# Performance work log

Measured on AMD Instinct MI355X. Metric: run time of the kernel, lower is better.

Reference implementation:

```python
import jax, jax.numpy as jnp
import numpy as np

B, L, V, D = 8, 2048, 1024, 512  # batch, seq (max_len), vocab_size (input feat), embedding_dim

def setup_inputs() -> dict:
    key = jax.random.key(0)
    kx, kq, kk, kv = jax.random.split(key, 4)
    scale = 1.0 / np.sqrt(V)
    return {
        "x": jax.random.normal(kx, (B, L, V), dtype=jnp.float32),
        "Wq": jax.random.uniform(kq, (D, V), dtype=jnp.float32, minval=-scale, maxval=scale),
        "Wk": jax.random.uniform(kk, (D, V), dtype=jnp.float32, minval=-scale, maxval=scale),
        "Wv": jax.random.uniform(kv, (D, V), dtype=jnp.float32, minval=-scale, maxval=scale),
    }

def reference(x, Wq, Wk, Wv):
    # nn.Linear without bias: y = x @ W.T
    q = jnp.einsum('blv,dv->bld', x, Wq)
    k = jnp.einsum('blv,dv->bld', x, Wk)
    v = jnp.einsum('blv,dv->bld', x, Wv)
    scores = jnp.einsum('bqd,bkd->bqk', q, k) / jnp.sqrt(jnp.float32(D))
    attn = jax.nn.softmax(scores, axis=2)
    return jnp.einsum('bqk,bkd->bqd', attn, v)
```

## Files before the change

### kernel.cpp

```cpp
#include <hip/hip_runtime.h>
#include <cstdint>
#include <cstddef>


typedef __attribute__((ext_vector_type(8))) __bf16 bf16x8;
typedef __attribute__((ext_vector_type(16))) float f32x16;
typedef __attribute__((ext_vector_type(4))) unsigned short ushort4v;
typedef __attribute__((ext_vector_type(4))) unsigned int uint4v;

__device__ __forceinline__ unsigned short f2bf(float f) {
  unsigned u = __float_as_uint(f);
  return (unsigned short)((u + 0x7fffu + ((u >> 16) & 1u)) >> 16);
}

__device__ __forceinline__ void async_load16(const unsigned short* g, unsigned short* l) {
  __builtin_amdgcn_global_load_lds(
      (__attribute__((address_space(1))) void*)(g),
      (__attribute__((address_space(3))) void*)(l), 16, 0, 0);
}

__global__ __launch_bounds__(256) void cvt_f32_bf16(const float* __restrict__ src,
                                                    unsigned short* __restrict__ dst) {
  int i = (blockIdx.x * 256 + threadIdx.x) * 4;
  float4 v = *(const float4*)(src + i);
  ushort4v o;
  o.x = f2bf(v.x); o.y = f2bf(v.y); o.z = f2bf(v.z); o.w = f2bf(v.w);
  *(ushort4v*)(dst + i) = o;
}

__global__ __launch_bounds__(256) void cvt_w3(const float* __restrict__ a,
                                              const float* __restrict__ b,
                                              const float* __restrict__ c,
                                              unsigned short* __restrict__ dst) {
  int bx = blockIdx.x;
  const float* src = (bx < 512) ? a : (bx < 1024) ? b : c;
  int seg = (bx < 512) ? 0 : (bx < 1024) ? 1 : 2;
  int i = ((bx & 511) * 256 + threadIdx.x) * 4;
  float4 v = *(const float4*)(src + i);
  ushort4v o;
  o.x = f2bf(v.x); o.y = f2bf(v.y); o.z = f2bf(v.z); o.w = f2bf(v.w);
  *(ushort4v*)(dst + seg * 524288 + i) = o;
}

__global__ __launch_bounds__(256) void gemm_qkv(
    const unsigned short* __restrict__ A0,
    const unsigned short* __restrict__ Bw,
    unsigned short* __restrict__ qk,
    unsigned short* __restrict__ vT) {
  __shared__ unsigned short sA[128 * 64];
  __shared__ unsigned short sB[128 * 64];
  const int tid = threadIdx.x;
  const int lane = tid & 63, wid = tid >> 6;
  const int wm = wid & 1, wn = wid >> 1;
  const int l31 = lane & 31, half = lane >> 5;

  int flat = blockIdx.x + blockIdx.y * 12;
  int sub = flat >> 3;
  int bxp = sub % 12;
  int byp = (flat & 7) * 16 + sub / 12;

  const unsigned short* A = A0 + (size_t)byp * 128 * 1024;
  const unsigned short* B = Bw + (size_t)bxp * 128 * 1024;

  f32x16 acc[2][2] = {};

  for (int k0 = 0; k0 < 1024; k0 += 64) {
    __syncthreads();
    #pragma unroll
    for (int p = 0; p < 4; ++p) {
      int u = p * 256 + tid;
      int r = u >> 3, cs = (u & 7) ^ (r & 7);
      async_load16(&A[(size_t)r * 1024 + k0 + cs * 8], &sA[u * 8]);
      async_load16(&B[(size_t)r * 1024 + k0 + cs * 8], &sB[u * 8]);
    }
    __syncthreads();

    #pragma unroll
    for (int ks = 0; ks < 4; ++ks) {
      int cb = ks * 2 + half;
      bf16x8 aF[2], bF[2];
      #pragma unroll
      for (int i = 0; i < 2; ++i) {
        int rA = wm * 64 + i * 32 + l31;
        aF[i] = *(const bf16x8*)&sA[(rA * 8 + (cb ^ (rA & 7))) * 8];
        int rB = wn * 64 + i * 32 + l31;
        bF[i] = *(const bf16x8*)&sB[(rB * 8 + (cb ^ (rB & 7))) * 8];
      }
      #pragma unroll
      for (int mt = 0; mt < 2; ++mt)
        #pragma unroll
        for (int nt = 0; nt < 2; ++nt)
          acc[mt][nt] = __builtin_amdgcn_mfma_f32_32x32x16_bf16(
              aF[mt], bF[nt], acc[mt][nt], 0, 0, 0);
    }
  }

  if (bxp < 8) {
    unsigned short* Cc = qk + (size_t)byp * 128 * 1024 + (size_t)bxp * 128;
    #pragma unroll
    for (int mt = 0; mt < 2; ++mt)
      #pragma unroll
      for (int nt = 0; nt < 2; ++nt) {
        int col = wn * 64 + nt * 32 + l31;
        #pragma unroll
        for (int q = 0; q < 4; ++q) {
          int row = wm * 64 + mt * 32 + half * 4 + q * 8;
          #pragma unroll
          for (int r2 = 0; r2 < 4; ++r2)
            Cc[(size_t)(row + r2) * 1024 + col] = f2bf(acc[mt][nt][q * 4 + r2]);
        }
      }
  } else {
    int nvx = bxp - 8;
    #pragma unroll
    for (int mt = 0; mt < 2; ++mt)
      #pragma unroll
      for (int nt = 0; nt < 2; ++nt) {
        int d = nvx * 128 + wn * 64 + nt * 32 + l31;
        #pragma unroll
        for (int q = 0; q < 4; ++q) {
          int grow = byp * 128 + wm * 64 + mt * 32 + half * 4 + q * 8;
          int b = grow >> 11, l = grow & 2047;
          ushort4v o;
          o.x = f2bf(acc[mt][nt][q * 4 + 0]); o.y = f2bf(acc[mt][nt][q * 4 + 1]);
          o.z = f2bf(acc[mt][nt][q * 4 + 2]); o.w = f2bf(acc[mt][nt][q * 4 + 3]);
          *(ushort4v*)&vT[(size_t)b * 1048576 + (size_t)d * 2048 + l] = o;
        }
      }
  }
}

__global__ __launch_bounds__(256) void gemm_exp(
    const unsigned short* __restrict__ qk,
    unsigned short* __restrict__ S, float scale) {
  __shared__ unsigned short sA[128 * 64];
  __shared__ unsigned short sB[128 * 64];
  const int tid = threadIdx.x;
  const int lane = tid & 63, wid = tid >> 6;
  const int wm = wid & 1, wn = wid >> 1;
  const int l31 = lane & 31, half = lane >> 5;

  int flat = blockIdx.x + (blockIdx.y << 4) + (blockIdx.z << 8);
  int z = flat & 7, rem = flat >> 3;
  int bxp = rem & 15, byp = rem >> 4;

  const unsigned short* A  = qk + (size_t)z * 2097152 + (size_t)byp * 128 * 1024;
  const unsigned short* Bk = qk + 512 + (size_t)z * 2097152 + (size_t)bxp * 128 * 1024;

  f32x16 acc[2][2] = {};

  for (int k0 = 0; k0 < 512; k0 += 64) {
    __syncthreads();
    #pragma unroll
    for (int p = 0; p < 4; ++p) {
      int u = p * 256 + tid;
      int r = u >> 3, cs = (u & 7) ^ (r & 7);
      async_load16(&A[(size_t)r * 1024 + k0 + cs * 8], &sA[u * 8]);
      async_load16(&Bk[(size_t)r * 1024 + k0 + cs * 8], &sB[u * 8]);
    }
    __syncthreads();

    #pragma unroll
    for (int ks = 0; ks < 4; ++ks) {
      int cb = ks * 2 + half;
      bf16x8 aF[2], bF[2];
      #pragma unroll
      for (int i = 0; i < 2; ++i) {
        int rA = wm * 64 + i * 32 + l31;
        aF[i] = *(const bf16x8*)&sA[(rA * 8 + (cb ^ (rA & 7))) * 8];
        int rB = wn * 64 + i * 32 + l31;
        bF[i] = *(const bf16x8*)&sB[(rB * 8 + (cb ^ (rB & 7))) * 8];
      }
      #pragma unroll
      for (int mt = 0; mt < 2; ++mt)
        #pragma unroll
        for (int nt = 0; nt < 2; ++nt)
          acc[mt][nt] = __builtin_amdgcn_mfma_f32_32x32x16_bf16(
              aF[mt], bF[nt], acc[mt][nt], 0, 0, 0);
    }
  }

  unsigned short* Cc = S + (size_t)z * 4194304 +
                       (size_t)byp * 128 * 2048 + (size_t)bxp * 128;
  #pragma unroll
  for (int mt = 0; mt < 2; ++mt)
    #pragma unroll
    for (int nt = 0; nt < 2; ++nt) {
      int col = wn * 64 + nt * 32 + l31;
      #pragma unroll
      for (int q = 0; q < 4; ++q) {
        int row = wm * 64 + mt * 32 + half * 4 + q * 8;
        #pragma unroll
        for (int r2 = 0; r2 < 4; ++r2)
          Cc[(size_t)(row + r2) * 2048 + col] =
              f2bf(__expf(acc[mt][nt][q * 4 + r2] * scale));
      }
    }
}

__global__ __launch_bounds__(256) void gemm_pvT(
    const unsigned short* __restrict__ S, const unsigned short* __restrict__ vT,
    float* __restrict__ out) {
  __shared__ unsigned short sA[128 * 64];
  __shared__ unsigned short sB[128 * 64];
  const int tid = threadIdx.x;
  const int lane = tid & 63, wid = tid >> 6;
  const int wm = wid & 1, wn = wid >> 1;
  const int l31 = lane & 31, half = lane >> 5;

  int flat = blockIdx.x + (blockIdx.y << 2) + (blockIdx.z << 6);
  int b = flat & 7, rem = flat >> 3;
  int dblk = rem & 3, qblk = rem >> 2;

  const unsigned short* A  = vT + (size_t)b * 1048576 + (size_t)dblk * 128 * 2048;
  const unsigned short* Bs = S  + (size_t)b * 4194304 + (size_t)qblk * 128 * 2048;

  f32x16 acc[2][2] = {};
  float rsum[2] = {0.f, 0.f};

  for (int k0 = 0; k0 < 2048; k0 += 64) {
    __syncthreads();
    #pragma unroll
    for (int p = 0; p < 4; ++p) {
      int u = p * 256 + tid;
      int r = u >> 3, cs = (u & 7) ^ (r & 7);
      async_load16(&A[(size_t)r * 2048 + k0 + cs * 8], &sA[u * 8]);
      async_load16(&Bs[(size_t)r * 2048 + k0 + cs * 8], &sB[u * 8]);
    }
    __syncthreads();

    #pragma unroll
    for (int ks = 0; ks < 4; ++ks) {
      int cb = ks * 2 + half;
      bf16x8 aF[2], bF[2];
      #pragma unroll
      for (int i = 0; i < 2; ++i) {
        int rA = wm * 64 + i * 32 + l31;
        aF[i] = *(const bf16x8*)&sA[(rA * 8 + (cb ^ (rA & 7))) * 8];
        int rB = wn * 64 + i * 32 + l31;
        bF[i] = *(const bf16x8*)&sB[(rB * 8 + (cb ^ (rB & 7))) * 8];
      }
      #pragma unroll
      for (int i = 0; i < 2; ++i) {
        uint4v u = __builtin_bit_cast(uint4v, bF[i]);
        #pragma unroll
        for (int t = 0; t < 4; ++t)
          rsum[i] += __uint_as_float(u[t] << 16) +
                     __uint_as_float(u[t] & 0xffff0000u);
      }
      #pragma unroll
      for (int mt = 0; mt < 2; ++mt)
        #pragma unroll
        for (int nt = 0; nt < 2; ++nt)
          acc[mt][nt] = __builtin_amdgcn_mfma_f32_32x32x16_bf16(
              aF[mt], bF[nt], acc[mt][nt], 0, 0, 0);
    }
  }

  #pragma unroll
  for (int i = 0; i < 2; ++i) rsum[i] += __shfl_xor(rsum[i], 32, 64);

  #pragma unroll
  for (int nt = 0; nt < 2; ++nt) {
    float inv = __builtin_amdgcn_rcpf(rsum[nt]);
    int qpos = qblk * 128 + wn * 64 + nt * 32 + l31;
    #pragma unroll
    for (int mt = 0; mt < 2; ++mt) {
      int d0 = dblk * 128 + wm * 64 + mt * 32 + half * 4;
      float* op = out + ((size_t)b * 2048 + qpos) * 512 + d0;
      #pragma unroll
      for (int q = 0; q < 4; ++q) {
        float4 o;
        o.x = acc[mt][nt][q * 4 + 0] * inv;
        o.y = acc[mt][nt][q * 4 + 1] * inv;
        o.z = acc[mt][nt][q * 4 + 2] * inv;
        o.w = acc[mt][nt][q * 4 + 3] * inv;
        *(float4*)(op + q * 8) = o;
      }
    }
  }
}

extern "C" void kernel_launch(void* const* d_in, const int* in_sizes, int n_in,
                              void* d_out, int out_size, void* d_ws, size_t ws_size,
                              hipStream_t stream) {
  const float* x  = (const float*)d_in[0];
  const float* Wq = (const float*)d_in[1];
  const float* Wk = (const float*)d_in[2];
  const float* Wv = (const float*)d_in[3];
  float* out = (float*)d_out;
  char* ws = (char*)d_ws;

  unsigned short* xb = (unsigned short*)ws;
  unsigned short* S  = (unsigned short*)ws;
  unsigned short* wf = (unsigned short*)(ws + 33554432);
  unsigned short* qk = (unsigned short*)(ws + 67108864);
  unsigned short* vT = (unsigned short*)(ws + 100663296);

  const float rsqrtD = 0.044194173824159216f;

  hipLaunchKernelGGL(cvt_f32_bf16, dim3(16384), dim3(256), 0, stream, x, xb);
  hipLaunchKernelGGL(cvt_w3, dim3(1536), dim3(256), 0, stream, Wq, Wk, Wv, wf);

  hipLaunchKernelGGL(gemm_qkv, dim3(12, 128, 1), dim3(256), 0, stream, xb, wf, qk, vT);

  hipLaunchKernelGGL(gemm_exp, dim3(16, 16, 8), dim3(256), 0, stream, qk, S, rsqrtD);

  hipLaunchKernelGGL(gemm_pvT, dim3(4, 16, 8), dim3(256), 0, stream, S, vT, out);

  (void)in_sizes; (void)n_in; (void)out_size; (void)ws_size;
}
```

Measured before the change: 267.6 us.

## Fuse all attention stages into one persistent cooperative kernel with grid syncs

Replaces the five separate launches (conversion, QKV GEMM, QK^T+exp, PV) with a single cooperative persistent kernel. Blocks loop over the tiles of each stage, with grid.sync between stages. The aim is to remove launch gaps and the tail effects between kernels. In exchange, the grid is capped at up to 768 blocks with launch_bounds(256,3), which may lower occupancy, and per-stage tiles are spread less evenly. The pvT stage has only 512 tiles, so some blocks sit idle there.

```diff
diff --git a/kernel.cpp b/kernel.cpp
--- a/kernel.cpp
+++ b/kernel.cpp
@@ -1,6 +1,9 @@
 #include <hip/hip_runtime.h>
+#include <hip/hip_cooperative_groups.h>
 #include <cstdint>
 #include <cstddef>
+
+namespace cg = cooperative_groups;
 
 
 typedef __attribute__((ext_vector_type(8))) __bf16 bf16x8;
@@ -18,6 +21,291 @@
       (__attribute__((address_space(1))) void*)(g),
       (__attribute__((address_space(3))) void*)(l), 16, 0, 0);
 }
+
+
+__device__ __forceinline__ void cvt_unit(int u0, const float* __restrict__ x,
+                                         const float* __restrict__ Wq,
+                                         const float* __restrict__ Wk,
+                                         const float* __restrict__ Wv,
+                                         unsigned short* __restrict__ xb,
+                                         unsigned short* __restrict__ wf, int tid) {
+  const float* src;
+  unsigned short* dst;
+  int i;
+  if (u0 < 16384) {
+    i = (u0 * 256 + tid) * 4;
+    src = x; dst = xb;
+  } else {
+    int bx = u0 - 16384;
+    src = (bx < 512) ? Wq : (bx < 1024) ? Wk : Wv;
+    int seg = (bx < 512) ? 0 : (bx < 1024) ? 1 : 2;
+    i = ((bx & 511) * 256 + tid) * 4;
+    dst = wf + seg * 524288;
+  }
+  float4 v = *(const float4*)(src + i);
+  ushort4v o;
+  o.x = f2bf(v.x); o.y = f2bf(v.y); o.z = f2bf(v.z); o.w = f2bf(v.w);
+  *(ushort4v*)(dst + i) = o;
+}
+
+__device__ __forceinline__ void qkv_tile(int flat, const unsigned short* __restrict__ A0,
+                                         const unsigned short* __restrict__ Bw,
+                                         unsigned short* __restrict__ qk,
+                                         unsigned short* __restrict__ vT,
+                                         unsigned short* sA, unsigned short* sB, int tid) {
+  const int lane = tid & 63, wid = tid >> 6;
+  const int wm = wid & 1, wn = wid >> 1;
+  const int l31 = lane & 31, half = lane >> 5;
+
+  int sub = flat >> 3;
+  int bxp = sub % 12;
+  int byp = (flat & 7) * 16 + sub / 12;
+
+  const unsigned short* A = A0 + (size_t)byp * 128 * 1024;
+  const unsigned short* B = Bw + (size_t)bxp * 128 * 1024;
+
+  f32x16 acc[2][2] = {};
+
+  for (int k0 = 0; k0 < 1024; k0 += 64) {
+    __syncthreads();
+    #pragma unroll
+    for (int p = 0; p < 4; ++p) {
+      int u = p * 256 + tid;
+      int r = u >> 3, cs = (u & 7) ^ (r & 7);
+      async_load16(&A[(size_t)r * 1024 + k0 + cs * 8], &sA[u * 8]);
+      async_load16(&B[(size_t)r * 1024 + k0 + cs * 8], &sB[u * 8]);
+    }
+    __syncthreads();
+
+    #pragma unroll
+    for (int ks = 0; ks < 4; ++ks) {
+      int cb = ks * 2 + half;
+      bf16x8 aF[2], bF[2];
+      #pragma unroll
+      for (int i = 0; i < 2; ++i) {
+        int rA = wm * 64 + i * 32 + l31;
+        aF[i] = *(const bf16x8*)&sA[(rA * 8 + (cb ^ (rA & 7))) * 8];
+        int rB = wn * 64 + i * 32 + l31;
+        bF[i] = *(const bf16x8*)&sB[(rB * 8 + (cb ^ (rB & 7))) * 8];
+      }
+      #pragma unroll
+      for (int mt = 0; mt < 2; ++mt)
+        #pragma unroll
+        for (int nt = 0; nt < 2; ++nt)
+          acc[mt][nt] = __builtin_amdgcn_mfma_f32_32x32x16_bf16(
+              aF[mt], bF[nt], acc[mt][nt], 0, 0, 0);
+    }
+  }
+
+  if (bxp < 8) {
+    unsigned short* Cc = qk + (size_t)byp * 128 * 1024 + (size_t)bxp * 128;
+    #pragma unroll
+    for (int mt = 0; mt < 2; ++mt)
+      #pragma unroll
+      for (int nt = 0; nt < 2; ++nt) {
+        int col = wn * 64 + nt * 32 + l31;
+        #pragma unroll
+        for (int q = 0; q < 4; ++q) {
+          int row = wm * 64 + mt * 32 + half * 4 + q * 8;
+          #pragma unroll
+          for (int r2 = 0; r2 < 4; ++r2)
+            Cc[(size_t)(row + r2) * 1024 + col] = f2bf(acc[mt][nt][q * 4 + r2]);
+        }
+      }
+  } else {
+    int nvx = bxp - 8;
+    #pragma unroll
+    for (int mt = 0; mt < 2; ++mt)
+      #pragma unroll
+      for (int nt = 0; nt < 2; ++nt) {
+        int d = nvx * 128 + wn * 64 + nt * 32 + l31;
+        #pragma unroll
+        for (int q = 0; q < 4; ++q) {
+          int grow = byp * 128 + wm * 64 + mt * 32 + half * 4 + q * 8;
+          int b = grow >> 11, l = grow & 2047;
+          ushort4v o;
+          o.x = f2bf(acc[mt][nt][q * 4 + 0]); o.y = f2bf(acc[mt][nt][q * 4 + 1]);
+          o.z = f2bf(acc[mt][nt][q * 4 + 2]); o.w = f2bf(acc[mt][nt][q * 4 + 3]);
+          *(ushort4v*)&vT[(size_t)b * 1048576 + (size_t)d * 2048 + l] = o;
+        }
+      }
+  }
+}
+
+__device__ __forceinline__ void exp_tile(int flat, const unsigned short* __restrict__ qk,
+                                         unsigned short* __restrict__ S,
+                                         unsigned short* sA, unsigned short* sB, int tid) {
+  const float scale = 0.044194173824159216f;
+  const int lane = tid & 63, wid = tid >> 6;
+  const int wm = wid & 1, wn = wid >> 1;
+  const int l31 = lane & 31, half = lane >> 5;
+
+  int z = flat & 7, rem = flat >> 3;
+  int bxp = rem & 15, byp = rem >> 4;
+
+  const unsigned short* A  = qk + (size_t)z * 2097152 + (size_t)byp * 128 * 1024;
+  const unsigned short* Bk = qk + 512 + (size_t)z * 2097152 + (size_t)bxp * 128 * 1024;
+
+  f32x16 acc[2][2] = {};
+
+  for (int k0 = 0; k0 < 512; k0 += 64) {
+    __syncthreads();
+    #pragma unroll
+    for (int p = 0; p < 4; ++p) {
+      int u = p * 256 + tid;
+      int r = u >> 3, cs = (u & 7) ^ (r & 7);
+      async_load16(&A[(size_t)r * 1024 + k0 + cs * 8], &sA[u * 8]);
+      async_load16(&Bk[(size_t)r * 1024 + k0 + cs * 8], &sB[u * 8]);
+    }
+    __syncthreads();
+
+    #pragma unroll
+    for (int ks = 0; ks < 4; ++ks) {
+      int cb = ks * 2 + half;
+      bf16x8 aF[2], bF[2];
+      #pragma unroll
+      for (int i = 0; i < 2; ++i) {
+        int rA = wm * 64 + i * 32 + l31;
+        aF[i] = *(const bf16x8*)&sA[(rA * 8 + (cb ^ (rA & 7))) * 8];
+        int rB = wn * 64 + i * 32 + l31;
+        bF[i] = *(const bf16x8*)&sB[(rB * 8 + (cb ^ (rB & 7))) * 8];
+      }
+      #pragma unroll
+      for (int mt = 0; mt < 2; ++mt)
+        #pragma unroll
+        for (int nt = 0; nt < 2; ++nt)
+          acc[mt][nt] = __builtin_amdgcn_mfma_f32_32x32x16_bf16(
+              aF[mt], bF[nt], acc[mt][nt], 0, 0, 0);
+    }
+  }
+
+  unsigned short* Cc = S + (size_t)z * 4194304 +
+                       (size_t)byp * 128 * 2048 + (size_t)bxp * 128;
+  #pragma unroll
+  for (int mt = 0; mt < 2; ++mt)
+    #pragma unroll
+    for (int nt = 0; nt < 2; ++nt) {
+      int col = wn * 64 + nt * 32 + l31;
+      #pragma unroll
+      for (int q = 0; q < 4; ++q) {
+        int row = wm * 64 + mt * 32 + half * 4 + q * 8;
+        #pragma unroll
+        for (int r2 = 0; r2 < 4; ++r2)
+          Cc[(size_t)(row + r2) * 2048 + col] =
+              f2bf(__expf(acc[mt][nt][q * 4 + r2] * scale));
+      }
+    }
+}
+
+__device__ __forceinline__ void pvT_tile(int flat, const unsigned short* __restrict__ S,
+                                         const unsigned short* __restrict__ vT,
+                                         float* __restrict__ out,
+                                         unsigned short* sA, unsigned short* sB, int tid) {
+  const int lane = tid & 63, wid = tid >> 6;
+  const int wm = wid & 1, wn = wid >> 1;
+  const int l31 = lane & 31, half = lane >> 5;
+
+  int b = flat & 7, rem = flat >> 3;
+  int dblk = rem & 3, qblk = rem >> 2;
+
+  const unsigned short* A  = vT + (size_t)b * 1048576 + (size_t)dblk * 128 * 2048;
+  const unsigned short* Bs = S  + (size_t)b * 4194304 + (size_t)qblk * 128 * 2048;
+
+  f32x16 acc[2][2] = {};
+  float rsum[2] = {0.f, 0.f};
+
+  for (int k0 = 0; k0 < 2048; k0 += 64) {
+    __syncthreads();
+    #pragma unroll
+    for (int p = 0; p < 4; ++p) {
+      int u = p * 256 + tid;
+      int r = u >> 3, cs = (u & 7) ^ (r & 7);
+      async_load16(&A[(size_t)r * 2048 + k0 + cs * 8], &sA[u * 8]);
+      async_load16(&Bs[(size_t)r * 2048 + k0 + cs * 8], &sB[u * 8]);
+    }
+    __syncthreads();
+
+    #pragma unroll
+    for (int ks = 0; ks < 4; ++ks) {
+      int cb = ks * 2 + half;
+      bf16x8 aF[2], bF[2];
+      #pragma unroll
+      for (int i = 0; i < 2; ++i) {
+        int rA = wm * 64 + i * 32 + l31;
+        aF[i] = *(const bf16x8*)&sA[(rA * 8 + (cb ^ (rA & 7))) * 8];
+        int rB = wn * 64 + i * 32 + l31;
+        bF[i] = *(const bf16x8*)&sB[(rB * 8 + (cb ^ (rB & 7))) * 8];
+      }
+      #pragma unroll
+      for (int i = 0; i < 2; ++i) {
+        uint4v u = __builtin_bit_cast(uint4v, bF[i]);
+        #pragma unroll
+        for (int t = 0; t < 4; ++t)
+          rsum[i] += __uint_as_float(u[t] << 16) +
+                     __uint_as_float(u[t] & 0xffff0000u);
+      }
+      #pragma unroll
+      for (int mt = 0; mt < 2; ++mt)
+        #pragma unroll
+        for (int nt = 0; nt < 2; ++nt)
+          acc[mt][nt] = __builtin_amdgcn_mfma_f32_32x32x16_bf16(
+              aF[mt], bF[nt], acc[mt][nt], 0, 0, 0);
+    }
+  }
+
+  #pragma unroll
+  for (int i = 0; i < 2; ++i) rsum[i] += __shfl_xor(rsum[i], 32, 64);
+
+  #pragma unroll
+  for (int nt = 0; nt < 2; ++nt) {
+    float inv = __builtin_amdgcn_rcpf(rsum[nt]);
+    int qpos = qblk * 128 + wn * 64 + nt * 32 + l31;
+    #pragma unroll
+    for (int mt = 0; mt < 2; ++mt) {
+      int d0 = dblk * 128 + wm * 64 + mt * 32 + half * 4;
+      float* op = out + ((size_t)b * 2048 + qpos) * 512 + d0;
+      #pragma unroll
+      for (int q = 0; q < 4; ++q) {
+        float4 o;
+        o.x = acc[mt][nt][q * 4 + 0] * inv;
+        o.y = acc[mt][nt][q * 4 + 1] * inv;
+        o.z = acc[mt][nt][q * 4 + 2] * inv;
+        o.w = acc[mt][nt][q * 4 + 3] * inv;
+        *(float4*)(op + q * 8) = o;
+      }
+    }
+  }
+}
+
+
+__global__ __launch_bounds__(256, 3) void fused_attn(
+    const float* __restrict__ x, const float* __restrict__ Wq,
+    const float* __restrict__ Wk, const float* __restrict__ Wv,
+    float* __restrict__ out, char* __restrict__ ws) {
+  __shared__ unsigned short sA[128 * 64];
+  __shared__ unsigned short sB[128 * 64];
+  unsigned short* xb = (unsigned short*)ws;
+  unsigned short* S  = (unsigned short*)ws;
+  unsigned short* wf = (unsigned short*)(ws + 33554432);
+  unsigned short* qk = (unsigned short*)(ws + 67108864);
+  unsigned short* vT = (unsigned short*)(ws + 100663296);
+  const int tid = threadIdx.x;
+  const int G = gridDim.x;
+  cg::grid_group grid = cg::this_grid();
+
+  for (int u = blockIdx.x; u < 17920; u += G)
+    cvt_unit(u, x, Wq, Wk, Wv, xb, wf, tid);
+  grid.sync();
+  for (int t = blockIdx.x; t < 1536; t += G)
+    qkv_tile(t, xb, wf, qk, vT, sA, sB, tid);
+  grid.sync();
+  for (int t = blockIdx.x; t < 2048; t += G)
+    exp_tile(t, qk, S, sA, sB, tid);
+  grid.sync();
+  for (int t = blockIdx.x; t < 512; t += G)
+    pvT_tile(t, S, vT, out, sA, sB, tid);
+}
+
 
 __global__ __launch_bounds__(256) void cvt_f32_bf16(const float* __restrict__ src,
                                                     unsigned short* __restrict__ dst) {
@@ -43,159 +331,18 @@
 }
 
 __global__ __launch_bounds__(256) void gemm_qkv(
-    const unsigned short* __restrict__ A0,
-    const unsigned short* __restrict__ Bw,
-    unsigned short* __restrict__ qk,
-    unsigned short* __restrict__ vT) {
+    const unsigned short* __restrict__ A0, const unsigned short* __restrict__ Bw,
+    unsigned short* __restrict__ qk, unsigned short* __restrict__ vT) {
   __shared__ unsigned short sA[128 * 64];
   __shared__ unsigned short sB[128 * 64];
-  const int tid = threadIdx.x;
-  const int lane = tid & 63, wid = tid >> 6;
-  const int wm = wid & 1, wn = wid >> 1;
-  const int l31 = lane & 31, half = lane >> 5;
-
-  int flat = blockIdx.x + blockIdx.y * 12;
-  int sub = flat >> 3;
-  int bxp = sub % 12;
-  int byp = (flat & 7) * 16 + sub / 12;
-
-  const unsigned short* A = A0 + (size_t)byp * 128 * 1024;
-  const unsigned short* B = Bw + (size_t)bxp * 128 * 1024;
-
-  f32x16 acc[2][2] = {};
-
-  for (int k0 = 0; k0 < 1024; k0 += 64) {
-    __syncthreads();
-    #pragma unroll
-    for (int p = 0; p < 4; ++p) {
-      int u = p * 256 + tid;
-      int r = u >> 3, cs = (u & 7) ^ (r & 7);
-      async_load16(&A[(size_t)r * 1024 + k0 + cs * 8], &sA[u * 8]);
-      async_load16(&B[(size_t)r * 1024 + k0 + cs * 8], &sB[u * 8]);
-    }
-    __syncthreads();
-
-    #pragma unroll
-    for (int ks = 0; ks < 4; ++ks) {
-      int cb = ks * 2 + half;
-      bf16x8 aF[2], bF[2];
-      #pragma unroll
-      for (int i = 0; i < 2; ++i) {
-        int rA = wm * 64 + i * 32 + l31;
-        aF[i] = *(const bf16x8*)&sA[(rA * 8 + (cb ^ (rA & 7))) * 8];
-        int rB = wn * 64 + i * 32 + l31;
-        bF[i] = *(const bf16x8*)&sB[(rB * 8 + (cb ^ (rB & 7))) * 8];
-      }
-      #pragma unroll
-      for (int mt = 0; mt < 2; ++mt)
-        #pragma unroll
-        for (int nt = 0; nt < 2; ++nt)
-          acc[mt][nt] = __builtin_amdgcn_mfma_f32_32x32x16_bf16(
-              aF[mt], bF[nt], acc[mt][nt], 0, 0, 0);
-    }
-  }
-
-  if (bxp < 8) {
-    unsigned short* Cc = qk + (size_t)byp * 128 * 1024 + (size_t)bxp * 128;
-    #pragma unroll
-    for (int mt = 0; mt < 2; ++mt)
-      #pragma unroll
-      for (int nt = 0; nt < 2; ++nt) {
-        int col = wn * 64 + nt * 32 + l31;
-        #pragma unroll
-        for (int q = 0; q < 4; ++q) {
-          int row = wm * 64 + mt * 32 + half * 4 + q * 8;
-          #pragma unroll
-          for (int r2 = 0; r2 < 4; ++r2)
-            Cc[(size_t)(row + r2) * 1024 + col] = f2bf(acc[mt][nt][q * 4 + r2]);
-        }
-      }
-  } else {
-    int nvx = bxp - 8;
-    #pragma unroll
-    for (int mt = 0; mt < 2; ++mt)
-      #pragma unroll
-      for (int nt = 0; nt < 2; ++nt) {
-        int d = nvx * 128 + wn * 64 + nt * 32 + l31;
-        #pragma unroll
-        for (int q = 0; q < 4; ++q) {
-          int grow = byp * 128 + wm * 64 + mt * 32 + half * 4 + q * 8;
-          int b = grow >> 11, l = grow & 2047;
-          ushort4v o;
-          o.x = f2bf(acc[mt][nt][q * 4 + 0]); o.y = f2bf(acc[mt][nt][q * 4 + 1]);
-          o.z = f2bf(acc[mt][nt][q * 4 + 2]); o.w = f2bf(acc[mt][nt][q * 4 + 3]);
-          *(ushort4v*)&vT[(size_t)b * 1048576 + (size_t)d * 2048 + l] = o;
-        }
-      }
-  }
+  qkv_tile(blockIdx.x + blockIdx.y * 12, A0, Bw, qk, vT, sA, sB, threadIdx.x);
 }
 
 __global__ __launch_bounds__(256) void gemm_exp(
-    const unsigned short* __restrict__ qk,
-    unsigned short* __restrict__ S, float scale) {
+    const unsigned short* __restrict__ qk, unsigned short* __restrict__ S) {
   __shared__ unsigned short sA[128 * 64];
   __shared__ unsigned short sB[128 * 64];
-  const int tid = threadIdx.x;
-  const int lane = tid & 63, wid = tid >> 6;
-  const int wm = wid & 1, wn = wid >> 1;
-  const int l31 = lane & 31, half = lane >> 5;
-
-  int flat = blockIdx.x + (blockIdx.y << 4) + (blockIdx.z << 8);
-  int z = flat & 7, rem = flat >> 3;
-  int bxp = rem & 15, byp = rem >> 4;
-
-  const unsigned short* A  = qk + (size_t)z * 2097152 + (size_t)byp * 128 * 1024;
-  const unsigned short* Bk = qk + 512 + (size_t)z * 2097152 + (size_t)bxp * 128 * 1024;
-
-  f32x16 acc[2][2] = {};
-
-  for (int k0 = 0; k0 < 512; k0 += 64) {
-    __syncthreads();
-    #pragma unroll
-    for (int p = 0; p < 4; ++p) {
-      int u = p * 256 + tid;
-      int r = u >> 3, cs = (u & 7) ^ (r & 7);
-      async_load16(&A[(size_t)r * 1024 + k0 + cs * 8], &sA[u * 8]);
-      async_load16(&Bk[(size_t)r * 1024 + k0 + cs * 8], &sB[u * 8]);
-    }
-    __syncthreads();
-
-    #pragma unroll
-    for (int ks = 0; ks < 4; ++ks) {
-      int cb = ks * 2 + half;
-      bf16x8 aF[2], bF[2];
-      #pragma unroll
-      for (int i = 0; i < 2; ++i) {
-        int rA = wm * 64 + i * 32 + l31;
-        aF[i] = *(const bf16x8*)&sA[(rA * 8 + (cb ^ (rA & 7))) * 8];
-        int rB = wn * 64 + i * 32 + l31;
-        bF[i] = *(const bf16x8*)&sB[(rB * 8 + (cb ^ (rB & 7))) * 8];
-      }
-      #pragma unroll
-      for (int mt = 0; mt < 2; ++mt)
-        #pragma unroll
-        for (int nt = 0; nt < 2; ++nt)
-          acc[mt][nt] = __builtin_amdgcn_mfma_f32_32x32x16_bf16(
-              aF[mt], bF[nt], acc[mt][nt], 0, 0, 0);
-    }
-  }
-
-  unsigned short* Cc = S + (size_t)z * 4194304 +
-                       (size_t)byp * 128 * 2048 + (size_t)bxp * 128;
-  #pragma unroll
-  for (int mt = 0; mt < 2; ++mt)
-    #pragma unroll
-    for (int nt = 0; nt < 2; ++nt) {
-      int col = wn * 64 + nt * 32 + l31;
-      #pragma unroll
-      for (int q = 0; q < 4; ++q) {
-        int row = wm * 64 + mt * 32 + half * 4 + q * 8;
-        #pragma unroll
-        for (int r2 = 0; r2 < 4; ++r2)
-          Cc[(size_t)(row + r2) * 2048 + col] =
-              f2bf(__expf(acc[mt][nt][q * 4 + r2] * scale));
-      }
-    }
+  exp_tile(blockIdx.x + (blockIdx.y << 4) + (blockIdx.z << 8), qk, S, sA, sB, threadIdx.x);
 }
 
 __global__ __launch_bounds__(256) void gemm_pvT(
@@ -203,82 +350,7 @@
     float* __restrict__ out) {
   __shared__ unsigned short sA[128 * 64];
   __shared__ unsigned short sB[128 * 64];
-  const int tid = threadIdx.x;
-  const int lane = tid & 63, wid = tid >> 6;
-  const int wm = wid & 1, wn = wid >> 1;
-  const int l31 = lane & 31, half = lane >> 5;
-
-  int flat = blockIdx.x + (blockIdx.y << 2) + (blockIdx.z << 6);
-  int b = flat & 7, rem = flat >> 3;
-  int dblk = rem & 3, qblk = rem >> 2;
-
-  const unsigned short* A  = vT + (size_t)b * 1048576 + (size_t)dblk * 128 * 2048;
-  const unsigned short* Bs = S  + (size_t)b * 4194304 + (size_t)qblk * 128 * 2048;
-
-  f32x16 acc[2][2] = {};
-  float rsum[2] = {0.f, 0.f};
-
-  for (int k0 = 0; k0 < 2048; k0 += 64) {
-    __syncthreads();
-    #pragma unroll
-    for (int p = 0; p < 4; ++p) {
-      int u = p * 256 + tid;
-      int r = u >> 3, cs = (u & 7) ^ (r & 7);
-      async_load16(&A[(size_t)r * 2048 + k0 + cs * 8], &sA[u * 8]);
-      async_load16(&Bs[(size_t)r * 2048 + k0 + cs * 8], &sB[u * 8]);
-    }
-    __syncthreads();
-
-    #pragma unroll
-    for (int ks = 0; ks < 4; ++ks) {
-      int cb = ks * 2 + half;
-      bf16x8 aF[2], bF[2];
-      #pragma unroll
-      for (int i = 0; i < 2; ++i) {
-        int rA = wm * 64 + i * 32 + l31;
-        aF[i] = *(const bf16x8*)&sA[(rA * 8 + (cb ^ (rA & 7))) * 8];
-        int rB = wn * 64 + i * 32 + l31;
-        bF[i] = *(const bf16x8*)&sB[(rB * 8 + (cb ^ (rB & 7))) * 8];
-      }
-      #pragma unroll
-      for (int i = 0; i < 2; ++i) {
-        uint4v u = __builtin_bit_cast(uint4v, bF[i]);
-        #pragma unroll
-        for (int t = 0; t < 4; ++t)
-          rsum[i] += __uint_as_float(u[t] << 16) +
-                     __uint_as_float(u[t] & 0xffff0000u);
-      }
-      #pragma unroll
-      for (int mt = 0; mt < 2; ++mt)
-        #pragma unroll
-        for (int nt = 0; nt < 2; ++nt)
-          acc[mt][nt] = __builtin_amdgcn_mfma_f32_32x32x16_bf16(
-              aF[mt], bF[nt], acc[mt][nt], 0, 0, 0);
-    }
-  }
-
-  #pragma unroll
-  for (int i = 0; i < 2; ++i) rsum[i] += __shfl_xor(rsum[i], 32, 64);
-
-  #pragma unroll
-  for (int nt = 0; nt < 2; ++nt) {
-    float inv = __builtin_amdgcn_rcpf(rsum[nt]);
-    int qpos = qblk * 128 + wn * 64 + nt * 32 + l31;
-    #pragma unroll
-    for (int mt = 0; mt < 2; ++mt) {
-      int d0 = dblk * 128 + wm * 64 + mt * 32 + half * 4;
-      float* op = out + ((size_t)b * 2048 + qpos) * 512 + d0;
-      #pragma unroll
-      for (int q = 0; q < 4; ++q) {
-        float4 o;
-        o.x = acc[mt][nt][q * 4 + 0] * inv;
-        o.y = acc[mt][nt][q * 4 + 1] * inv;
-        o.z = acc[mt][nt][q * 4 + 2] * inv;
-        o.w = acc[mt][nt][q * 4 + 3] * inv;
-        *(float4*)(op + q * 8) = o;
-      }
-    }
-  }
+  pvT_tile(blockIdx.x + (blockIdx.y << 2) + (blockIdx.z << 6), S, vT, out, sA, sB, threadIdx.x);
 }
 
 extern "C" void kernel_launch(void* const* d_in, const int* in_sizes, int n_in,
@@ -297,16 +369,34 @@
   unsigned short* qk = (unsigned short*)(ws + 67108864);
   unsigned short* vT = (unsigned short*)(ws + 100663296);
 
-  const float rsqrtD = 0.044194173824159216f;
-
-  hipLaunchKernelGGL(cvt_f32_bf16, dim3(16384), dim3(256), 0, stream, x, xb);
-  hipLaunchKernelGGL(cvt_w3, dim3(1536), dim3(256), 0, stream, Wq, Wk, Wv, wf);
-
-  hipLaunchKernelGGL(gemm_qkv, dim3(12, 128, 1), dim3(256), 0, stream, xb, wf, qk, vT);
-
-  hipLaunchKernelGGL(gemm_exp, dim3(16, 16, 8), dim3(256), 0, stream, qk, S, rsqrtD);
-
-  hipLaunchKernelGGL(gemm_pvT, dim3(4, 16, 8), dim3(256), 0, stream, S, vT, out);
+  static int coopGrid = -2;
+  if (coopGrid == -2) {
+    int nb = 0;
+    hipError_t e = hipOccupancyMaxActiveBlocksPerMultiprocessor(&nb, fused_attn, 256, 0);
+    if (e == hipSuccess && nb >= 1)
+      coopGrid = (nb * 256 < 768) ? nb * 256 : 768;
+    else
+      coopGrid = -1;
+  }
+
+  bool done = false;
+  if (coopGrid > 0) {
+    void* args[] = {(void*)&x, (void*)&Wq, (void*)&Wk, (void*)&Wv,
+                    (void*)&out, (void*)&ws};
+    hipError_t e = hipLaunchCooperativeKernel((const void*)fused_attn,
+                                              dim3(coopGrid), dim3(256),
+                                              args, 0, stream);
+    if (e == hipSuccess) done = true;
+    else coopGrid = -1;
+  }
+
+  if (!done) {
+    hipLaunchKernelGGL(cvt_f32_bf16, dim3(16384), dim3(256), 0, stream, x, xb);
+    hipLaunchKernelGGL(cvt_w3, dim3(1536), dim3(256), 0, stream, Wq, Wk, Wv, wf);
+    hipLaunchKernelGGL(gemm_qkv, dim3(12, 128, 1), dim3(256), 0, stream, xb, wf, qk, vT);
+    hipLaunchKernelGGL(gemm_exp, dim3(16, 16, 8), dim3(256), 0, stream, qk, S);
+    hipLaunchKernelGGL(gemm_pvT, dim3(4, 16, 8), dim3(256), 0, stream, S, vT, out);
+  }
 
   (void)in_sizes; (void)n_in; (void)out_size; (void)ws_size;
 }
```

New measurement: 551.4 us. +106.0%, slower.

## Enlarge GEMM tiles to 256x128 and merge conversion kernels into one launch

Applied to the files above, without the earlier changes.

All three GEMM kernels move from a 128x128 to a 256x128 block tile, with each wave computing a 4x2 set of MFMA accumulators. This raises arithmetic intensity per LDS load and cuts global reloads of the B operand. The two fp32-to-bf16 conversion kernels are merged into one launch, and grids are flattened to 1D. The trade-off is fewer blocks (only 256 for the PV GEMM, roughly one per CU), more registers and more LDS per block, which can lower occupancy and latency hiding.

```diff
diff --git a/kernel.cpp b/kernel.cpp
--- a/kernel.cpp
+++ b/kernel.cpp
@@ -19,58 +19,65 @@
       (__attribute__((address_space(3))) void*)(l), 16, 0, 0);
 }
 
-__global__ __launch_bounds__(256) void cvt_f32_bf16(const float* __restrict__ src,
-                                                    unsigned short* __restrict__ dst) {
-  int i = (blockIdx.x * 256 + threadIdx.x) * 4;
+__global__ __launch_bounds__(256) void cvt_all(
+    const float* __restrict__ x, const float* __restrict__ Wq,
+    const float* __restrict__ Wk, const float* __restrict__ Wv,
+    unsigned short* __restrict__ xb, unsigned short* __restrict__ wf) {
+  int u0 = blockIdx.x, tid = threadIdx.x;
+  const float* src;
+  unsigned short* dst;
+  int i;
+  if (u0 < 16384) {
+    i = (u0 * 256 + tid) * 4;
+    src = x; dst = xb;
+  } else {
+    int bx = u0 - 16384;
+    src = (bx < 512) ? Wq : (bx < 1024) ? Wk : Wv;
+    int seg = (bx < 512) ? 0 : (bx < 1024) ? 1 : 2;
+    i = ((bx & 511) * 256 + tid) * 4;
+    dst = wf + seg * 524288;
+  }
   float4 v = *(const float4*)(src + i);
   ushort4v o;
   o.x = f2bf(v.x); o.y = f2bf(v.y); o.z = f2bf(v.z); o.w = f2bf(v.w);
   *(ushort4v*)(dst + i) = o;
 }
 
-__global__ __launch_bounds__(256) void cvt_w3(const float* __restrict__ a,
-                                              const float* __restrict__ b,
-                                              const float* __restrict__ c,
-                                              unsigned short* __restrict__ dst) {
-  int bx = blockIdx.x;
-  const float* src = (bx < 512) ? a : (bx < 1024) ? b : c;
-  int seg = (bx < 512) ? 0 : (bx < 1024) ? 1 : 2;
-  int i = ((bx & 511) * 256 + threadIdx.x) * 4;
-  float4 v = *(const float4*)(src + i);
-  ushort4v o;
-  o.x = f2bf(v.x); o.y = f2bf(v.y); o.z = f2bf(v.z); o.w = f2bf(v.w);
-  *(ushort4v*)(dst + seg * 524288 + i) = o;
-}
-
-__global__ __launch_bounds__(256) void gemm_qkv(
+
+__global__ __launch_bounds__(256, 3) void gemm_qkv(
     const unsigned short* __restrict__ A0,
     const unsigned short* __restrict__ Bw,
     unsigned short* __restrict__ qk,
     unsigned short* __restrict__ vT) {
-  __shared__ unsigned short sA[128 * 64];
+  __shared__ unsigned short sA[256 * 64];
   __shared__ unsigned short sB[128 * 64];
   const int tid = threadIdx.x;
   const int lane = tid & 63, wid = tid >> 6;
   const int wm = wid & 1, wn = wid >> 1;
   const int l31 = lane & 31, half = lane >> 5;
 
-  int flat = blockIdx.x + blockIdx.y * 12;
+  int flat = blockIdx.x;
   int sub = flat >> 3;
   int bxp = sub % 12;
-  int byp = (flat & 7) * 16 + sub / 12;
-
-  const unsigned short* A = A0 + (size_t)byp * 128 * 1024;
+  int byp = (flat & 7) * 8 + sub / 12;
+
+  const unsigned short* A = A0 + (size_t)byp * 256 * 1024;
   const unsigned short* B = Bw + (size_t)bxp * 128 * 1024;
 
-  f32x16 acc[2][2] = {};
+  f32x16 acc[4][2] = {};
 
   for (int k0 = 0; k0 < 1024; k0 += 64) {
     __syncthreads();
     #pragma unroll
+    for (int p = 0; p < 8; ++p) {
+      int u = p * 256 + tid;
+      int r = u >> 3, cs = (u & 7) ^ (r & 7);
+      async_load16(&A[(size_t)r * 1024 + k0 + cs * 8], &sA[u * 8]);
+    }
+    #pragma unroll
     for (int p = 0; p < 4; ++p) {
       int u = p * 256 + tid;
       int r = u >> 3, cs = (u & 7) ^ (r & 7);
-      async_load16(&A[(size_t)r * 1024 + k0 + cs * 8], &sA[u * 8]);
       async_load16(&B[(size_t)r * 1024 + k0 + cs * 8], &sB[u * 8]);
     }
     __syncthreads();
@@ -78,33 +85,34 @@
     #pragma unroll
     for (int ks = 0; ks < 4; ++ks) {
       int cb = ks * 2 + half;
-      bf16x8 aF[2], bF[2];
+      bf16x8 bF[2];
       #pragma unroll
       for (int i = 0; i < 2; ++i) {
-        int rA = wm * 64 + i * 32 + l31;
-        aF[i] = *(const bf16x8*)&sA[(rA * 8 + (cb ^ (rA & 7))) * 8];
         int rB = wn * 64 + i * 32 + l31;
         bF[i] = *(const bf16x8*)&sB[(rB * 8 + (cb ^ (rB & 7))) * 8];
       }
       #pragma unroll
-      for (int mt = 0; mt < 2; ++mt)
+      for (int mt = 0; mt < 4; ++mt) {
+        int rA = wm * 128 + mt * 32 + l31;
+        bf16x8 aF = *(const bf16x8*)&sA[(rA * 8 + (cb ^ (rA & 7))) * 8];
         #pragma unroll
         for (int nt = 0; nt < 2; ++nt)
           acc[mt][nt] = __builtin_amdgcn_mfma_f32_32x32x16_bf16(
-              aF[mt], bF[nt], acc[mt][nt], 0, 0, 0);
+              aF, bF[nt], acc[mt][nt], 0, 0, 0);
+      }
     }
   }
 
   if (bxp < 8) {
-    unsigned short* Cc = qk + (size_t)byp * 128 * 1024 + (size_t)bxp * 128;
-    #pragma unroll
-    for (int mt = 0; mt < 2; ++mt)
+    unsigned short* Cc = qk + (size_t)byp * 256 * 1024 + (size_t)bxp * 128;
+    #pragma unroll
+    for (int mt = 0; mt < 4; ++mt)
       #pragma unroll
       for (int nt = 0; nt < 2; ++nt) {
         int col = wn * 64 + nt * 32 + l31;
         #pragma unroll
         for (int q = 0; q < 4; ++q) {
-          int row = wm * 64 + mt * 32 + half * 4 + q * 8;
+          int row = wm * 128 + mt * 32 + half * 4 + q * 8;
           #pragma unroll
           for (int r2 = 0; r2 < 4; ++r2)
             Cc[(size_t)(row + r2) * 1024 + col] = f2bf(acc[mt][nt][q * 4 + r2]);
@@ -113,13 +121,13 @@
   } else {
     int nvx = bxp - 8;
     #pragma unroll
-    for (int mt = 0; mt < 2; ++mt)
+    for (int mt = 0; mt < 4; ++mt)
       #pragma unroll
       for (int nt = 0; nt < 2; ++nt) {
         int d = nvx * 128 + wn * 64 + nt * 32 + l31;
         #pragma unroll
         for (int q = 0; q < 4; ++q) {
-          int grow = byp * 128 + wm * 64 + mt * 32 + half * 4 + q * 8;
+          int grow = byp * 256 + wm * 128 + mt * 32 + half * 4 + q * 8;
           int b = grow >> 11, l = grow & 2047;
           ushort4v o;
           o.x = f2bf(acc[mt][nt][q * 4 + 0]); o.y = f2bf(acc[mt][nt][q * 4 + 1]);
@@ -130,32 +138,38 @@
   }
 }
 
-__global__ __launch_bounds__(256) void gemm_exp(
+__global__ __launch_bounds__(256, 3) void gemm_exp(
     const unsigned short* __restrict__ qk,
-    unsigned short* __restrict__ S, float scale) {
-  __shared__ unsigned short sA[128 * 64];
+    unsigned short* __restrict__ S) {
+  const float scale = 0.044194173824159216f;
+  __shared__ unsigned short sA[256 * 64];
   __shared__ unsigned short sB[128 * 64];
   const int tid = threadIdx.x;
   const int lane = tid & 63, wid = tid >> 6;
   const int wm = wid & 1, wn = wid >> 1;
   const int l31 = lane & 31, half = lane >> 5;
 
-  int flat = blockIdx.x + (blockIdx.y << 4) + (blockIdx.z << 8);
+  int flat = blockIdx.x;
   int z = flat & 7, rem = flat >> 3;
   int bxp = rem & 15, byp = rem >> 4;
 
-  const unsigned short* A  = qk + (size_t)z * 2097152 + (size_t)byp * 128 * 1024;
+  const unsigned short* A  = qk + (size_t)z * 2097152 + (size_t)byp * 256 * 1024;
   const unsigned short* Bk = qk + 512 + (size_t)z * 2097152 + (size_t)bxp * 128 * 1024;
 
-  f32x16 acc[2][2] = {};
+  f32x16 acc[4][2] = {};
 
   for (int k0 = 0; k0 < 512; k0 += 64) {
     __syncthreads();
     #pragma unroll
+    for (int p = 0; p < 8; ++p) {
+      int u = p * 256 + tid;
+      int r = u >> 3, cs = (u & 7) ^ (r & 7);
+      async_load16(&A[(size_t)r * 1024 + k0 + cs * 8], &sA[u * 8]);
+    }
+    #pragma unroll
     for (int p = 0; p < 4; ++p) {
       int u = p * 256 + tid;
       int r = u >> 3, cs = (u & 7) ^ (r & 7);
-      async_load16(&A[(size_t)r * 1024 + k0 + cs * 8], &sA[u * 8]);
       async_load16(&Bk[(size_t)r * 1024 + k0 + cs * 8], &sB[u * 8]);
     }
     __syncthreads();
@@ -163,33 +177,34 @@
     #pragma unroll
     for (int ks = 0; ks < 4; ++ks) {
       int cb = ks * 2 + half;
-      bf16x8 aF[2], bF[2];
+      bf16x8 bF[2];
       #pragma unroll
       for (int i = 0; i < 2; ++i) {
-        int rA = wm * 64 + i * 32 + l31;
-        aF[i] = *(const bf16x8*)&sA[(rA * 8 + (cb ^ (rA & 7))) * 8];
         int rB = wn * 64 + i * 32 + l31;
         bF[i] = *(const bf16x8*)&sB[(rB * 8 + (cb ^ (rB & 7))) * 8];
       }
       #pragma unroll
-      for (int mt = 0; mt < 2; ++mt)
+      for (int mt = 0; mt < 4; ++mt) {
+        int rA = wm * 128 + mt * 32 + l31;
+        bf16x8 aF = *(const bf16x8*)&sA[(rA * 8 + (cb ^ (rA & 7))) * 8];
         #pragma unroll
         for (int nt = 0; nt < 2; ++nt)
           acc[mt][nt] = __builtin_amdgcn_mfma_f32_32x32x16_bf16(
-              aF[mt], bF[nt], acc[mt][nt], 0, 0, 0);
+              aF, bF[nt], acc[mt][nt], 0, 0, 0);
+      }
     }
   }
 
   unsigned short* Cc = S + (size_t)z * 4194304 +
-                       (size_t)byp * 128 * 2048 + (size_t)bxp * 128;
+                       (size_t)byp * 256 * 2048 + (size_t)bxp * 128;
   #pragma unroll
-  for (int mt = 0; mt < 2; ++mt)
+  for (int mt = 0; mt < 4; ++mt)
     #pragma unroll
     for (int nt = 0; nt < 2; ++nt) {
       int col = wn * 64 + nt * 32 + l31;
       #pragma unroll
       for (int q = 0; q < 4; ++q) {
-        int row = wm * 64 + mt * 32 + half * 4 + q * 8;
+        int row = wm * 128 + mt * 32 + half * 4 + q * 8;
         #pragma unroll
         for (int r2 = 0; r2 < 4; ++r2)
           Cc[(size_t)(row + r2) * 2048 + col] =
@@ -198,33 +213,38 @@
     }
 }
 
-__global__ __launch_bounds__(256) void gemm_pvT(
+__global__ __launch_bounds__(256, 2) void gemm_pvT(
     const unsigned short* __restrict__ S, const unsigned short* __restrict__ vT,
     float* __restrict__ out) {
-  __shared__ unsigned short sA[128 * 64];
+  __shared__ unsigned short sA[256 * 64];
   __shared__ unsigned short sB[128 * 64];
   const int tid = threadIdx.x;
   const int lane = tid & 63, wid = tid >> 6;
   const int wm = wid & 1, wn = wid >> 1;
   const int l31 = lane & 31, half = lane >> 5;
 
-  int flat = blockIdx.x + (blockIdx.y << 2) + (blockIdx.z << 6);
+  int flat = blockIdx.x;
   int b = flat & 7, rem = flat >> 3;
-  int dblk = rem & 3, qblk = rem >> 2;
-
-  const unsigned short* A  = vT + (size_t)b * 1048576 + (size_t)dblk * 128 * 2048;
+  int dblk = rem & 1, qblk = rem >> 1;
+
+  const unsigned short* A  = vT + (size_t)b * 1048576 + (size_t)dblk * 256 * 2048;
   const unsigned short* Bs = S  + (size_t)b * 4194304 + (size_t)qblk * 128 * 2048;
 
-  f32x16 acc[2][2] = {};
+  f32x16 acc[4][2] = {};
   float rsum[2] = {0.f, 0.f};
 
   for (int k0 = 0; k0 < 2048; k0 += 64) {
     __syncthreads();
     #pragma unroll
+    for (int p = 0; p < 8; ++p) {
+      int u = p * 256 + tid;
+      int r = u >> 3, cs = (u & 7) ^ (r & 7);
+      async_load16(&A[(size_t)r * 2048 + k0 + cs * 8], &sA[u * 8]);
+    }
+    #pragma unroll
     for (int p = 0; p < 4; ++p) {
       int u = p * 256 + tid;
       int r = u >> 3, cs = (u & 7) ^ (r & 7);
-      async_load16(&A[(size_t)r * 2048 + k0 + cs * 8], &sA[u * 8]);
       async_load16(&Bs[(size_t)r * 2048 + k0 + cs * 8], &sB[u * 8]);
     }
     __syncthreads();
@@ -232,11 +252,9 @@
     #pragma unroll
     for (int ks = 0; ks < 4; ++ks) {
       int cb = ks * 2 + half;
-      bf16x8 aF[2], bF[2];
+      bf16x8 bF[2];
       #pragma unroll
       for (int i = 0; i < 2; ++i) {
-        int rA = wm * 64 + i * 32 + l31;
-        aF[i] = *(const bf16x8*)&sA[(rA * 8 + (cb ^ (rA & 7))) * 8];
         int rB = wn * 64 + i * 32 + l31;
         bF[i] = *(const bf16x8*)&sB[(rB * 8 + (cb ^ (rB & 7))) * 8];
       }
@@ -249,11 +267,14 @@
                      __uint_as_float(u[t] & 0xffff0000u);
       }
       #pragma unroll
-      for (int mt = 0; mt < 2; ++mt)
+      for (int mt = 0; mt < 4; ++mt) {
+        int rA = wm * 128 + mt * 32 + l31;
+        bf16x8 aF = *(const bf16x8*)&sA[(rA * 8 + (cb ^ (rA & 7))) * 8];
         #pragma unroll
         for (int nt = 0; nt < 2; ++nt)
           acc[mt][nt] = __builtin_amdgcn_mfma_f32_32x32x16_bf16(
-              aF[mt], bF[nt], acc[mt][nt], 0, 0, 0);
+              aF, bF[nt], acc[mt][nt], 0, 0, 0);
+      }
     }
   }
 
@@ -265,8 +286,8 @@
     float inv = __builtin_amdgcn_rcpf(rsum[nt]);
     int qpos = qblk * 128 + wn * 64 + nt * 32 + l31;
     #pragma unroll
-    for (int mt = 0; mt < 2; ++mt) {
-      int d0 = dblk * 128 + wm * 64 + mt * 32 + half * 4;
+    for (int mt = 0; mt < 4; ++mt) {
+      int d0 = dblk * 256 + wm * 128 + mt * 32 + half * 4;
       float* op = out + ((size_t)b * 2048 + qpos) * 512 + d0;
       #pragma unroll
       for (int q = 0; q < 4; ++q) {
@@ -297,16 +318,14 @@
   unsigned short* qk = (unsigned short*)(ws + 67108864);
   unsigned short* vT = (unsigned short*)(ws + 100663296);
 
-  const float rsqrtD = 0.044194173824159216f;
-
-  hipLaunchKernelGGL(cvt_f32_bf16, dim3(16384), dim3(256), 0, stream, x, xb);
-  hipLaunchKernelGGL(cvt_w3, dim3(1536), dim3(256), 0, stream, Wq, Wk, Wv, wf);
-
-  hipLaunchKernelGGL(gemm_qkv, dim3(12, 128, 1), dim3(256), 0, stream, xb, wf, qk, vT);
-
-  hipLaunchKernelGGL(gemm_exp, dim3(16, 16, 8), dim3(256), 0, stream, qk, S, rsqrtD);
-
-  hipLaunchKernelGGL(gemm_pvT, dim3(4, 16, 8), dim3(256), 0, stream, S, vT, out);
+  hipLaunchKernelGGL(cvt_all, dim3(17920), dim3(256), 0, stream,
+                     x, Wq, Wk, Wv, xb, wf);
+
+  hipLaunchKernelGGL(gemm_qkv, dim3(768), dim3(256), 0, stream, xb, wf, qk, vT);
+
+  hipLaunchKernelGGL(gemm_exp, dim3(1024), dim3(256), 0, stream, qk, S);
+
+  hipLaunchKernelGGL(gemm_pvT, dim3(256), dim3(256), 0, stream, S, vT, out);
 
   (void)in_sizes; (void)n_in; (void)out_size; (void)ws_size;
 }
```

Measured after the change: 318.9 us. 1.19x slower.
